# Optimization experiments

Measured on AMD Instinct MI355X. Metric: run time of the kernel, lower is better.

The kernel has to match this reference:

```python
import jax, jax.numpy as jnp
import numpy as np

N, D, H, E = 50000, 128, 128, 800000

def _layernorm(h, g, b, eps=1e-5):
    m = jnp.mean(h, axis=-1, keepdims=True)
    v = jnp.mean((h - m) ** 2, axis=-1, keepdims=True)
    return (h - m) * jax.lax.rsqrt(v + eps) * g + b

def setup_inputs() -> dict:
    key = jax.random.key(0)
    ks = jax.random.split(key, 24)
    s = 0.02
    inp = {
        "x": jax.random.normal(ks[0], (N, D), dtype=jnp.float32),
        "edge_index": jax.random.randint(ks[1], (2, E), 0, N, dtype=jnp.int64),
        "degree": jax.random.uniform(ks[2], (N, 1), dtype=jnp.float32) * 32.0,
        "W_lin": jax.random.normal(ks[3], (D, H), jnp.float32) * s,
        "b_lin": jnp.zeros((H,), jnp.float32),
        "Wa1": jax.random.normal(ks[4], (H, H), jnp.float32) * s,
        "ba1": jnp.zeros((H,), jnp.float32),
        "Wa2": jax.random.normal(ks[5], (H, H), jnp.float32) * s,
        "ba2": jnp.zeros((H,), jnp.float32),
        "Wb1": jax.random.normal(ks[6], (H, H), jnp.float32) * s,
        "bb1": jnp.zeros((H,), jnp.float32),
        "Wb2": jax.random.normal(ks[7], (H, H), jnp.float32) * s,
        "bb2": jnp.zeros((H,), jnp.float32),
        "Wg1": jax.random.normal(ks[8], (H, H), jnp.float32) * s,
        "bg1": jnp.zeros((H,), jnp.float32),
        "Wg2": jax.random.normal(ks[9], (H, H), jnp.float32) * s,
        "bg2": jnp.zeros((H,), jnp.float32),
        "Wf1": jax.random.normal(ks[10], (H, H), jnp.float32) * s,
        "bf1": jnp.zeros((H,), jnp.float32),
        "Wf2": jax.random.normal(ks[11], (H, H), jnp.float32) * s,
        "bf2": jnp.zeros((H,), jnp.float32),
        "ln_g": jnp.ones((H,), jnp.float32),
        "ln_b": jnp.zeros((H,), jnp.float32),
    }
    return inp

def reference(x, edge_index, degree, W_lin, b_lin, Wa1, ba1, Wa2, ba2,
              Wb1, bb1, Wb2, bb2, Wg1, bg1, Wg2, bg2, Wf1, bf1, Wf2, bf2,
              ln_g, ln_b):
    # Dropout layers are identity (eval mode)
    h = x @ W_lin + b_lin                                  # [N,H]
    x_res = _layernorm(h, ln_g, ln_b)
    alpha = jax.nn.softplus(jax.nn.relu(h @ Wa1 + ba1) @ Wa2 + ba2)
    beta = jax.nn.softplus(jax.nn.relu(h @ Wb1 + bb1) @ Wb2 + bb2)
    gamma = jax.nn.gelu(h @ Wg1 + bg1, approximate=False) @ Wg2 + bg2
    src, dst = edge_index[0], edge_index[1]
    agg = jax.ops.segment_sum(h[src], dst, num_segments=h.shape[0])  # [N,H]
    y = (beta * agg + gamma) / (alpha + beta * degree)
    z = jax.nn.gelu(y @ Wf1 + bf1, approximate=False) @ Wf2 + bf2
    return z + x_res
```

## Files before the change

### kernel.cpp

```cpp
#include <hip/hip_runtime.h>
#include <hip/hip_bf16.h>
#include <math.h>

#define NODES 50000
#define NEDGE 800000
#define NT_TILES 782
#define NBUCK 98
#define BSHIFT 9
#define BCAP 10240
#define NP1 195
#define EPB1 4104

typedef __bf16 bf16_t;
typedef __bf16 bf16x8 __attribute__((ext_vector_type(8)));
typedef float floatx4 __attribute__((ext_vector_type(4)));

__device__ __forceinline__ float bfbits2f(unsigned int hi16) {
    union { unsigned int u; float f; } c; c.u = hi16; return c.f;
}
__device__ __forceinline__ unsigned short f2bfbits(float f) {
    bf16_t b = (bf16_t)f; unsigned short u;
    __builtin_memcpy(&u, &b, 2); return u;
}

__device__ __forceinline__ float act_rt(float v, int act) {
    if (act == 1) return fmaxf(v, 0.f);
    if (act == 2) {
        float w = 0.79788456f * (v + 0.044715f * v * v * v);
        float e = __expf(2.f * w);
        float th = 1.f - 2.f / (e + 1.f);
        return 0.5f * v * (1.f + th);
    }
    if (act == 3) return fmaxf(v, 0.f) + __logf(1.f + __expf(-fabsf(v)));
    return v;
}

__global__ __launch_bounds__(256) void prep_w_zero(
    const float* __restrict__ w0, const float* __restrict__ w1,
    const float* __restrict__ w2, const float* __restrict__ w3,
    const float* __restrict__ w4, const float* __restrict__ w5,
    const float* __restrict__ w6, const float* __restrict__ w7,
    const float* __restrict__ w8, bf16_t* __restrict__ wt,
    int* __restrict__ gcur)
{
    if (blockIdx.x >= 9) {
        if (threadIdx.x < NBUCK) gcur[threadIdx.x] = 0;
        return;
    }
    const float* Ws[9] = {w0, w1, w2, w3, w4, w5, w6, w7, w8};
    const float* W = Ws[blockIdx.x];
    bf16_t* o = wt + blockIdx.x * 16384;
    for (int idx = threadIdx.x; idx < 16384; idx += 256) {
        int k = idx >> 7, n = idx & 127;
        o[n * 128 + k] = (bf16_t)W[idx];
    }
}

__device__ __forceinline__ void load_w_regs(const bf16_t* __restrict__ W,
                                            uint4 (&wr)[8], int t)
{
    for (int i = 0; i < 8; ++i) {
        int c = t + i * 256;
        int row = c >> 4, g = c & 15;
        wr[i] = *(const uint4*)(W + row * 128 + g * 8);
    }
}
__device__ __forceinline__ void store_w_regs(const uint4 (&wr)[8],
                                             bf16_t* Bs, int t)
{
    for (int i = 0; i < 8; ++i) {
        int c = t + i * 256;
        int row = c >> 4, g = c & 15;
        *(uint4*)&Bs[row * 128 + ((g ^ (row & 15)) * 8)] = wr[i];
    }
}
__device__ __forceinline__ void afrag_gbf16(const bf16_t* __restrict__ A,
        bf16x8 (&af)[4], int r0, int lane, int wave, int M)
{
    int gr = r0 + wave * 16 + (lane & 15);
    gr = min(gr, M - 1);
    const bf16_t* p = A + (size_t)gr * 128 + (lane >> 4) * 8;
    for (int kc = 0; kc < 4; ++kc)
        af[kc] = *(const bf16x8*)(p + kc * 32);
}
__device__ __forceinline__ void kloop64(const bf16x8 (&af)[4], const bf16_t* Bs,
                                        floatx4 (&acc)[8], int l15, int quad)
{
    for (int ni = 0; ni < 8; ++ni)
        for (int r = 0; r < 4; ++r) acc[ni][r] = 0.f;
    for (int kc = 0; kc < 4; ++kc) {
        int kg = kc * 4 + quad;
        bf16x8 b[8];
        for (int ni = 0; ni < 8; ++ni) {
            int row = ni * 16 + l15;
            b[ni] = *(const bf16x8*)&Bs[row * 128 + ((kg ^ l15) * 8)];
        }
        for (int ni = 0; ni < 8; ++ni)
            acc[ni] = __builtin_amdgcn_mfma_f32_16x16x32_bf16(
                af[kc], b[ni], acc[ni], 0, 0, 0);
    }
}
__device__ __forceinline__ void write_Csw(bf16_t* Csw, floatx4 (&acc)[8],
        const float (&bias_r)[8], int lane, int wave, int act)
{
    const int l15 = lane & 15, quad = lane >> 4;
    for (int ni = 0; ni < 8; ++ni) {
        int col = ni * 16 + l15;
        for (int r = 0; r < 4; ++r) {
            int row = wave * 16 + quad * 4 + r;
            float v = act_rt(acc[ni][r] + bias_r[ni], act);
            Csw[row * 128 + (((col >> 3) ^ (row & 15)) << 3) + (col & 7)] = (bf16_t)v;
        }
    }
}
__device__ __forceinline__ void afrag_Csw(const bf16_t* Csw, bf16x8 (&af)[4],
                                          int lane, int wave)
{
    int l15 = lane & 15, quad = lane >> 4;
    int row = wave * 16 + l15;
    for (int kc = 0; kc < 4; ++kc) {
        int kg = kc * 4 + quad;
        af[kc] = *(const bf16x8*)&Csw[row * 128 + ((kg ^ l15) * 8)];
    }
}
__device__ __forceinline__ void copy_Csw_out(const bf16_t* Csw,
        bf16_t* __restrict__ out, int t, int r0, int M)
{
    for (int i = 0; i < 4; ++i) {
        int c = t + i * 256;
        int row = c >> 4, g = c & 15;
        int gr = r0 + row;
        if (gr < M)
            *(uint4*)(out + (size_t)gr * 128 + g * 8) =
                *(const uint4*)&Csw[row * 128 + ((g ^ (row & 15)) * 8)];
    }
}

__global__ __launch_bounds__(256, 3) void hln_p1(
    const float* __restrict__ x, const bf16_t* __restrict__ wt,
    const float* __restrict__ b_lin,
    const float* __restrict__ ln_g, const float* __restrict__ ln_b,
    bf16_t* __restrict__ h, bf16_t* __restrict__ xres,
    const int* __restrict__ ei, int* __restrict__ gcur,
    unsigned* __restrict__ ebuf, int M)
{
    __shared__ __align__(16) char smem[49152];
    const int t = threadIdx.x;
    const int bid = blockIdx.x;

    if (bid % 5 == 4) {
        int* lcnt  = (int*)smem;
        int* lbase = lcnt + NBUCK;
        if (t < NBUCK) lcnt[t] = 0;
        __syncthreads();
        int p1id = bid / 5;
        int base = p1id * EPB1;
        int e_end = min(base + EPB1, NEDGE);
        for (int e = base + t; e < e_end; e += 256)
            atomicAdd(&lcnt[ei[NEDGE + e] >> BSHIFT], 1);
        __syncthreads();
        if (t < NBUCK) {
            lbase[t] = atomicAdd(&gcur[t], lcnt[t]);
            lcnt[t] = 0;
        }
        __syncthreads();
        for (int e = base + t; e < e_end; e += 256) {
            int d = ei[NEDGE + e];
            int s = ei[e];
            int b = d >> BSHIFT;
            int off = atomicAdd(&lcnt[b], 1);
            int pos = lbase[b] + off;
            if (pos < BCAP)
                ebuf[(size_t)b * BCAP + pos] =
                    (unsigned)s | ((unsigned)(d & 511) << 16);
        }
        return;
    }

    bf16_t* Bs  = (bf16_t*)smem;
    bf16_t* Csw = (bf16_t*)(smem + 32768);
    const int tile = bid - bid / 5;
    const int r0 = tile * 64;
    const int lane = t & 63, wave = t >> 6, l15 = lane & 15, quad = lane >> 4;
    uint4 wr[8];
    bf16x8 af[4];
    floatx4 acc[8];
    float bias_r[8];
    for (int ni = 0; ni < 8; ++ni) bias_r[ni] = b_lin[ni * 16 + l15];

    {
        int gr = min(r0 + wave * 16 + l15, M - 1);
        const float* p = x + (size_t)gr * 128 + quad * 8;
        for (int kc = 0; kc < 4; ++kc) {
            float4 u0 = *(const float4*)(p + kc * 32);
            float4 u1 = *(const float4*)(p + kc * 32 + 4);
            bf16x8 f;
            f[0] = (bf16_t)u0.x; f[1] = (bf16_t)u0.y;
            f[2] = (bf16_t)u0.z; f[3] = (bf16_t)u0.w;
            f[4] = (bf16_t)u1.x; f[5] = (bf16_t)u1.y;
            f[6] = (bf16_t)u1.z; f[7] = (bf16_t)u1.w;
            af[kc] = f;
        }
    }
    load_w_regs(wt, wr, t);
    store_w_regs(wr, Bs, t);
    __syncthreads();
    kloop64(af, Bs, acc, l15, quad);
    write_Csw(Csw, acc, bias_r, lane, wave, 0);
    __syncthreads();

    int row = t >> 2, p4 = t & 3;
    int gr = r0 + row;
    uint4 raw[4];
    float vals[32];
    float s = 0.f, sq = 0.f;
    for (int i = 0; i < 4; ++i) {
        int lg = p4 * 4 + i;
        raw[i] = *(const uint4*)&Csw[row * 128 + ((lg ^ (row & 15)) * 8)];
        const unsigned* u = (const unsigned*)&raw[i];
        for (int k = 0; k < 4; ++k) {
            float f0 = bfbits2f(u[k] << 16);
            float f1 = bfbits2f(u[k] & 0xffff0000u);
            vals[i * 8 + k * 2] = f0; vals[i * 8 + k * 2 + 1] = f1;
            s += f0 + f1; sq += f0 * f0 + f1 * f1;
        }
    }
    s += __shfl_xor(s, 1, 64);  sq += __shfl_xor(sq, 1, 64);
    s += __shfl_xor(s, 2, 64);  sq += __shfl_xor(sq, 2, 64);
    float m   = s * (1.f / 128.f);
    float var = fmaxf(sq * (1.f / 128.f) - m * m, 0.f);
    float rs  = rsqrtf(var + 1e-5f);
    if (gr < M) {
        for (int i = 0; i < 4; ++i) {
            int lg = p4 * 4 + i;
            *(uint4*)(h + (size_t)gr * 128 + lg * 8) = raw[i];
            unsigned short ob[8];
            for (int k = 0; k < 8; ++k) {
                int col = lg * 8 + k;
                ob[k] = f2bfbits((vals[i * 8 + k] - m) * rs * ln_g[col] + ln_b[col]);
            }
            uint4 o;
            o.x = ob[0] | ((unsigned)ob[1] << 16);
            o.y = ob[2] | ((unsigned)ob[3] << 16);
            o.z = ob[4] | ((unsigned)ob[5] << 16);
            o.w = ob[6] | ((unsigned)ob[7] << 16);
            *(uint4*)(xres + (size_t)gr * 128 + lg * 8) = o;
        }
    }
}

__global__ __launch_bounds__(256, 3) void branch_all(
    const bf16_t* __restrict__ h, const bf16_t* __restrict__ wt,
    const float* __restrict__ ba1, const float* __restrict__ ba2,
    const float* __restrict__ bb1, const float* __restrict__ bb2,
    const float* __restrict__ bg1, const float* __restrict__ bg2,
    bf16_t* __restrict__ al, bf16_t* __restrict__ be, bf16_t* __restrict__ ga,
    const int* __restrict__ gcur, const unsigned* __restrict__ ebuf,
    int* __restrict__ off_start, int* __restrict__ cntN,
    int* __restrict__ srcs, int M)
{
    __shared__ __align__(16) char smem[49152];
    const int t = threadIdx.x;
    const int bid = blockIdx.x;

    if (bid % 9 == 8) {
        int* ncnt = (int*)smem;
        int* sa   = ncnt + 512;
        int* sb   = sa + 512;
        int* ncur = sb + 512;
        int* red  = ncur + 512;
        const int b = bid / 9;
        if (b >= NBUCK) return;
        int total = min(gcur[b], BCAP);

        int v = 0;
        for (int j = t; j < b; j += 256) v += min(gcur[j], BCAP);
        for (int o = 1; o < 64; o <<= 1) v += __shfl_xor(v, o, 64);
        if ((t & 63) == 0) red[t >> 6] = v;
        ncnt[t] = 0; ncnt[t + 256] = 0;
        __syncthreads();
        int bucketBase = red[0] + red[1] + red[2] + red[3];

        const unsigned* eb = ebuf + (size_t)b * BCAP;
        for (int i = t; i < total; i += 256)
            atomicAdd(&ncnt[eb[i] >> 16], 1);
        __syncthreads();
        sa[t] = ncnt[t]; sa[t + 256] = ncnt[t + 256];
        __syncthreads();
        int* pin = sa; int* pout = sb;
        for (int o = 1; o < 512; o <<= 1) {
            for (int j = t; j < 512; j += 256)
                pout[j] = pin[j] + (j >= o ? pin[j - o] : 0);
            __syncthreads();
            int* tmp = pin; pin = pout; pout = tmp;
        }
        for (int j = t; j < 512; j += 256) {
            int excl = pin[j] - ncnt[j];
            int node = (b << BSHIFT) + j;
            if (node < NODES) {
                off_start[node] = bucketBase + excl;
                cntN[node] = ncnt[j];
            }
            ncur[j] = excl;
        }
        __syncthreads();
        for (int i = t; i < total; i += 256) {
            unsigned p = eb[i];
            int dl = p >> 16;
            int pos = atomicAdd(&ncur[dl], 1);
            srcs[bucketBase + pos] = (int)(p & 0xFFFFu);
        }
        return;
    }

    const int tile = bid - bid / 9;
    if (tile >= NT_TILES) return;
    bf16_t* Bs  = (bf16_t*)smem;
    bf16_t* Csw = (bf16_t*)(smem + 32768);
    const int r0 = tile * 64;
    const int lane = t & 63, wave = t >> 6, l15 = lane & 15, quad = lane >> 4;
    uint4 wr[8];
    bf16x8 af_h[4], af_t[4];
    floatx4 acc[8];
    float b1_r[8], b2_r[8];

    const float* B1s[3] = {ba1, bb1, bg1};
    const float* B2s[3] = {ba2, bb2, bg2};
    bf16_t* outs[3] = {al, be, ga};
    const int act1s[3] = {1, 1, 2};
    const int act2s[3] = {3, 3, 0};

    afrag_gbf16(h, af_h, r0, lane, wave, M);
    load_w_regs(wt + 1 * 16384, wr, t);

    #pragma unroll
    for (int b = 0; b < 3; ++b) {
        store_w_regs(wr, Bs, t);
        load_w_regs(wt + (2 + 2 * b) * 16384, wr, t);
        for (int ni = 0; ni < 8; ++ni) {
            b1_r[ni] = B1s[b][ni * 16 + l15];
            b2_r[ni] = B2s[b][ni * 16 + l15];
        }
        __syncthreads();
        kloop64(af_h, Bs, acc, l15, quad);
        write_Csw(Csw, acc, b1_r, lane, wave, act1s[b]);
        __syncthreads();
        store_w_regs(wr, Bs, t);
        afrag_Csw(Csw, af_t, lane, wave);
        if (b < 2)
            load_w_regs(wt + (3 + 2 * b) * 16384, wr, t);
        __syncthreads();
        kloop64(af_t, Bs, acc, l15, quad);
        __syncthreads();
        write_Csw(Csw, acc, b2_r, lane, wave, act2s[b]);
        __syncthreads();
        copy_Csw_out(Csw, outs[b], t, r0, M);
    }
}

__global__ __launch_bounds__(256) void gather_y_kernel(
    const int* __restrict__ off_start, const int* __restrict__ cnt,
    const int* __restrict__ srcs, const bf16_t* __restrict__ h,
    const bf16_t* __restrict__ al, const bf16_t* __restrict__ be,
    const bf16_t* __restrict__ ga, const float* __restrict__ deg,
    bf16_t* __restrict__ y, int M)
{
    int wave = threadIdx.x >> 6, lane = threadIdx.x & 63;
    int node = blockIdx.x * 4 + wave;
    if (node >= M) return;
    int s0 = __builtin_amdgcn_readfirstlane(off_start[node]);
    int n  = __builtin_amdgcn_readfirstlane(cnt[node]);
    int grp = lane >> 4, c16 = lane & 15;
    float a[8] = {0.f, 0.f, 0.f, 0.f, 0.f, 0.f, 0.f, 0.f};

    for (int j = 0; j < n; j += 16) {
        int idx[4];
        #pragma unroll
        for (int s = 0; s < 4; ++s)
            idx[s] = srcs[s0 + min(j + 4 * s + grp, n - 1)];
        uint4 v[4];
        #pragma unroll
        for (int s = 0; s < 4; ++s)
            v[s] = *(const uint4*)(h + (size_t)idx[s] * 128 + c16 * 8);
        #pragma unroll
        for (int s = 0; s < 4; ++s) {
            if (j + 4 * s + grp < n) {
                const unsigned* u = (const unsigned*)&v[s];
                #pragma unroll
                for (int k = 0; k < 4; ++k) {
                    a[2 * k]     += bfbits2f(u[k] << 16);
                    a[2 * k + 1] += bfbits2f(u[k] & 0xffff0000u);
                }
            }
        }
    }
    for (int k = 0; k < 8; ++k) {
        a[k] += __shfl_xor(a[k], 16, 64);
        a[k] += __shfl_xor(a[k], 32, 64);
    }
    if (lane < 16) {
        size_t i0 = (size_t)node * 128 + (size_t)c16 * 8;
        uint4 ra = *(const uint4*)(al + i0);
        uint4 rb = *(const uint4*)(be + i0);
        uint4 rg = *(const uint4*)(ga + i0);
        float d = deg[node];
        const unsigned* ua = (const unsigned*)&ra;
        const unsigned* ub = (const unsigned*)&rb;
        const unsigned* ug = (const unsigned*)&rg;
        unsigned short o[8];
        for (int k = 0; k < 4; ++k) {
            float a0 = bfbits2f(ua[k] << 16), a1 = bfbits2f(ua[k] & 0xffff0000u);
            float b0 = bfbits2f(ub[k] << 16), b1 = bfbits2f(ub[k] & 0xffff0000u);
            float g0 = bfbits2f(ug[k] << 16), g1 = bfbits2f(ug[k] & 0xffff0000u);
            o[2 * k]     = f2bfbits((b0 * a[2 * k]     + g0) / (a0 + b0 * d));
            o[2 * k + 1] = f2bfbits((b1 * a[2 * k + 1] + g1) / (a1 + b1 * d));
        }
        uint4 ov;
        ov.x = o[0] | ((unsigned)o[1] << 16);
        ov.y = o[2] | ((unsigned)o[3] << 16);
        ov.z = o[4] | ((unsigned)o[5] << 16);
        ov.w = o[6] | ((unsigned)o[7] << 16);
        *(uint4*)(y + i0) = ov;
    }
}

__global__ __launch_bounds__(256, 3) void fused_out(
    const bf16_t* __restrict__ y, const bf16_t* __restrict__ wt,
    const float* __restrict__ bf1, const float* __restrict__ bf2,
    const bf16_t* __restrict__ xres, float* __restrict__ out, int M)
{
    __shared__ __align__(16) char smem[49152];
    bf16_t* Bs  = (bf16_t*)smem;
    bf16_t* Csw = (bf16_t*)(smem + 32768);
    float*  Cf  = (float*)smem;
    const int t = threadIdx.x;
    const int r0 = blockIdx.x * 64;
    const int lane = t & 63, wave = t >> 6, l15 = lane & 15, quad = lane >> 4;
    uint4 wr[8];
    bf16x8 af[4];
    floatx4 acc[8];

    float b1_r[8], b2_r[8];
    for (int ni = 0; ni < 8; ++ni) {
        b1_r[ni] = bf1[ni * 16 + l15];
        b2_r[ni] = bf2[ni * 16 + l15];
    }

    afrag_gbf16(y, af, r0, lane, wave, M);
    load_w_regs(wt + 7 * 16384, wr, t);
    store_w_regs(wr, Bs, t);
    load_w_regs(wt + 8 * 16384, wr, t);
    __syncthreads();

    kloop64(af, Bs, acc, l15, quad);
    write_Csw(Csw, acc, b1_r, lane, wave, 2);
    __syncthreads();
    store_w_regs(wr, Bs, t);
    __syncthreads();

    afrag_Csw(Csw, af, lane, wave);
    kloop64(af, Bs, acc, l15, quad);
    __syncthreads();

    for (int ni = 0; ni < 8; ++ni) {
        int col = ni * 16 + l15;
        for (int r = 0; r < 4; ++r) {
            int row = wave * 16 + quad * 4 + r;
            Cf[row * 132 + col] = acc[ni][r] + b2_r[ni];
        }
    }
    __syncthreads();
    for (int i = 0; i < 8; ++i) {
        int c = t + i * 256;
        int row = c >> 5, q = c & 31;
        int gr = r0 + row;
        if (gr < M) {
            float4 v = *(const float4*)&Cf[row * 132 + q * 4];
            uint2 xr = *(const uint2*)(xres + (size_t)gr * 128 + q * 4);
            v.x += bfbits2f(xr.x << 16);
            v.y += bfbits2f(xr.x & 0xffff0000u);
            v.z += bfbits2f(xr.y << 16);
            v.w += bfbits2f(xr.y & 0xffff0000u);
            *(float4*)(out + (size_t)gr * 128 + q * 4) = v;
        }
    }
}

extern "C" void kernel_launch(void* const* d_in, const int* in_sizes, int n_in,
                              void* d_out, int out_size, void* d_ws, size_t ws_size,
                              hipStream_t stream)
{
    const float* x    = (const float*)d_in[0];
    const int*   ei   = (const int*)d_in[1];
    const float* deg  = (const float*)d_in[2];
    const float* W_lin = (const float*)d_in[3];  const float* b_lin = (const float*)d_in[4];
    const float* Wa1 = (const float*)d_in[5];    const float* ba1 = (const float*)d_in[6];
    const float* Wa2 = (const float*)d_in[7];    const float* ba2 = (const float*)d_in[8];
    const float* Wb1 = (const float*)d_in[9];    const float* bb1 = (const float*)d_in[10];
    const float* Wb2 = (const float*)d_in[11];   const float* bb2 = (const float*)d_in[12];
    const float* Wg1 = (const float*)d_in[13];   const float* bg1 = (const float*)d_in[14];
    const float* Wg2 = (const float*)d_in[15];   const float* bg2 = (const float*)d_in[16];
    const float* Wf1 = (const float*)d_in[17];   const float* bf1 = (const float*)d_in[18];
    const float* Wf2 = (const float*)d_in[19];   const float* bf2 = (const float*)d_in[20];
    const float* ln_g = (const float*)d_in[21];  const float* ln_b = (const float*)d_in[22];

    const int M = NODES;
    const size_t NB2 = (size_t)M * 128 * 2;

    char* ws = (char*)d_ws;
    size_t off = 0;
    bf16_t* wt  = (bf16_t*)(ws + off); off += (size_t)9 * 16384 * 2;
    bf16_t* h   = (bf16_t*)(ws + off); off += NB2;
    bf16_t* al  = (bf16_t*)(ws + off); off += NB2;
    bf16_t* be  = (bf16_t*)(ws + off); off += NB2;
    bf16_t* ga  = (bf16_t*)(ws + off); off += NB2;
    bf16_t* yv  = (bf16_t*)(ws + off); off += NB2;
    bf16_t* xres = (bf16_t*)(ws + off); off += NB2;
    int* gcur      = (int*)(ws + off); off += 128 * 4;
    int* off_start = (int*)(ws + off); off += (size_t)NODES * 4 + 64;
    int* cntN      = (int*)(ws + off); off += (size_t)NODES * 4 + 64;
    int* srcs      = (int*)(ws + off); off += (size_t)NEDGE * 4;
    unsigned* ebuf = (unsigned*)(ws + off); off += (size_t)NBUCK * BCAP * 4;
    float* outp = (float*)d_out;

    dim3 blk(256);

    prep_w_zero<<<10, blk, 0, stream>>>(
        W_lin, Wa1, Wa2, Wb1, Wb2, Wg1, Wg2, Wf1, Wf2, wt, gcur);

    hln_p1<<<977, blk, 0, stream>>>(
        x, wt, b_lin, ln_g, ln_b, h, xres, ei, gcur, ebuf, M);

    branch_all<<<891, blk, 0, stream>>>(
        h, wt, ba1, ba2, bb1, bb2, bg1, bg2, al, be, ga,
        gcur, ebuf, off_start, cntN, srcs, M);

    gather_y_kernel<<<(M + 3) / 4, blk, 0, stream>>>(off_start, cntN, srcs, h,
                                                     al, be, ga, deg, yv, M);
    fused_out<<<NT_TILES, blk, 0, stream>>>(yv, wt, bf1, bf2, xres, outp, M);
}
```

Before: 289.5 us.

## Read MFMA weight fragments directly from global memory instead of LDS staging

```diff
diff --git a/kernel.cpp b/kernel.cpp
--- a/kernel.cpp
+++ b/kernel.cpp
@@ -56,45 +56,31 @@
     }
 }
 
-__device__ __forceinline__ void load_w_regs(const bf16_t* __restrict__ W,
-                                            uint4 (&wr)[8], int t)
-{
-    for (int i = 0; i < 8; ++i) {
-        int c = t + i * 256;
-        int row = c >> 4, g = c & 15;
-        wr[i] = *(const uint4*)(W + row * 128 + g * 8);
-    }
-}
-__device__ __forceinline__ void store_w_regs(const uint4 (&wr)[8],
-                                             bf16_t* Bs, int t)
-{
-    for (int i = 0; i < 8; ++i) {
-        int c = t + i * 256;
-        int row = c >> 4, g = c & 15;
-        *(uint4*)&Bs[row * 128 + ((g ^ (row & 15)) * 8)] = wr[i];
-    }
-}
 __device__ __forceinline__ void afrag_gbf16(const bf16_t* __restrict__ A,
         bf16x8 (&af)[4], int r0, int lane, int wave, int M)
 {
     int gr = r0 + wave * 16 + (lane & 15);
     gr = min(gr, M - 1);
     const bf16_t* p = A + (size_t)gr * 128 + (lane >> 4) * 8;
+    #pragma unroll
     for (int kc = 0; kc < 4; ++kc)
         af[kc] = *(const bf16x8*)(p + kc * 32);
 }
-__device__ __forceinline__ void kloop64(const bf16x8 (&af)[4], const bf16_t* Bs,
-                                        floatx4 (&acc)[8], int l15, int quad)
-{
+__device__ __forceinline__ void kloop64g(const bf16x8 (&af)[4],
+        const bf16_t* __restrict__ W, floatx4 (&acc)[8], int l15, int quad)
+{
+    #pragma unroll
     for (int ni = 0; ni < 8; ++ni)
+        #pragma unroll
         for (int r = 0; r < 4; ++r) acc[ni][r] = 0.f;
+    #pragma unroll
     for (int kc = 0; kc < 4; ++kc) {
         int kg = kc * 4 + quad;
         bf16x8 b[8];
-        for (int ni = 0; ni < 8; ++ni) {
-            int row = ni * 16 + l15;
-            b[ni] = *(const bf16x8*)&Bs[row * 128 + ((kg ^ l15) * 8)];
-        }
+        #pragma unroll
+        for (int ni = 0; ni < 8; ++ni)
+            b[ni] = *(const bf16x8*)(W + (ni * 16 + l15) * 128 + kg * 8);
+        #pragma unroll
         for (int ni = 0; ni < 8; ++ni)
             acc[ni] = __builtin_amdgcn_mfma_f32_16x16x32_bf16(
                 af[kc], b[ni], acc[ni], 0, 0, 0);
@@ -104,8 +90,10 @@
         const float (&bias_r)[8], int lane, int wave, int act)
 {
     const int l15 = lane & 15, quad = lane >> 4;
+    #pragma unroll
     for (int ni = 0; ni < 8; ++ni) {
         int col = ni * 16 + l15;
+        #pragma unroll
         for (int r = 0; r < 4; ++r) {
             int row = wave * 16 + quad * 4 + r;
             float v = act_rt(acc[ni][r] + bias_r[ni], act);
@@ -118,6 +106,7 @@
 {
     int l15 = lane & 15, quad = lane >> 4;
     int row = wave * 16 + l15;
+    #pragma unroll
     for (int kc = 0; kc < 4; ++kc) {
         int kg = kc * 4 + quad;
         af[kc] = *(const bf16x8*)&Csw[row * 128 + ((kg ^ l15) * 8)];
@@ -126,6 +115,7 @@
 __device__ __forceinline__ void copy_Csw_out(const bf16_t* Csw,
         bf16_t* __restrict__ out, int t, int r0, int M)
 {
+    #pragma unroll
     for (int i = 0; i < 4; ++i) {
         int c = t + i * 256;
         int row = c >> 4, g = c & 15;
@@ -136,7 +126,7 @@
     }
 }
 
-__global__ __launch_bounds__(256, 3) void hln_p1(
+__global__ __launch_bounds__(256, 4) void hln_p1(
     const float* __restrict__ x, const bf16_t* __restrict__ wt,
     const float* __restrict__ b_lin,
     const float* __restrict__ ln_g, const float* __restrict__ ln_b,
@@ -144,7 +134,7 @@
     const int* __restrict__ ei, int* __restrict__ gcur,
     unsigned* __restrict__ ebuf, int M)
 {
-    __shared__ __align__(16) char smem[49152];
+    __shared__ __align__(16) char smem[16384];
     const int t = threadIdx.x;
     const int bid = blockIdx.x;
 
@@ -177,12 +167,10 @@
         return;
     }
 
-    bf16_t* Bs  = (bf16_t*)smem;
-    bf16_t* Csw = (bf16_t*)(smem + 32768);
+    bf16_t* Csw = (bf16_t*)smem;
     const int tile = bid - bid / 5;
     const int r0 = tile * 64;
     const int lane = t & 63, wave = t >> 6, l15 = lane & 15, quad = lane >> 4;
-    uint4 wr[8];
     bf16x8 af[4];
     floatx4 acc[8];
     float bias_r[8];
@@ -191,6 +179,7 @@
     {
         int gr = min(r0 + wave * 16 + l15, M - 1);
         const float* p = x + (size_t)gr * 128 + quad * 8;
+        #pragma unroll
         for (int kc = 0; kc < 4; ++kc) {
             float4 u0 = *(const float4*)(p + kc * 32);
             float4 u1 = *(const float4*)(p + kc * 32 + 4);
@@ -202,10 +191,7 @@
             af[kc] = f;
         }
     }
-    load_w_regs(wt, wr, t);
-    store_w_regs(wr, Bs, t);
-    __syncthreads();
-    kloop64(af, Bs, acc, l15, quad);
+    kloop64g(af, wt, acc, l15, quad);
     write_Csw(Csw, acc, bias_r, lane, wave, 0);
     __syncthreads();
 
@@ -249,7 +235,7 @@
     }
 }
 
-__global__ __launch_bounds__(256, 3) void branch_all(
+__global__ __launch_bounds__(256, 4) void branch_all(
     const bf16_t* __restrict__ h, const bf16_t* __restrict__ wt,
     const float* __restrict__ ba1, const float* __restrict__ ba2,
     const float* __restrict__ bb1, const float* __restrict__ bb2,
@@ -259,7 +245,7 @@
     int* __restrict__ off_start, int* __restrict__ cntN,
     int* __restrict__ srcs, int M)
 {
-    __shared__ __align__(16) char smem[49152];
+    __shared__ __align__(16) char smem[16384];
     const int t = threadIdx.x;
     const int bid = blockIdx.x;
 
@@ -315,11 +301,9 @@
 
     const int tile = bid - bid / 9;
     if (tile >= NT_TILES) return;
-    bf16_t* Bs  = (bf16_t*)smem;
-    bf16_t* Csw = (bf16_t*)(smem + 32768);
+    bf16_t* Csw = (bf16_t*)smem;
     const int r0 = tile * 64;
     const int lane = t & 63, wave = t >> 6, l15 = lane & 15, quad = lane >> 4;
-    uint4 wr[8];
     bf16x8 af_h[4], af_t[4];
     floatx4 acc[8];
     float b1_r[8], b2_r[8];
@@ -331,30 +315,21 @@
     const int act2s[3] = {3, 3, 0};
 
     afrag_gbf16(h, af_h, r0, lane, wave, M);
-    load_w_regs(wt + 1 * 16384, wr, t);
 
     #pragma unroll
     for (int b = 0; b < 3; ++b) {
-        store_w_regs(wr, Bs, t);
-        load_w_regs(wt + (2 + 2 * b) * 16384, wr, t);
         for (int ni = 0; ni < 8; ++ni) {
             b1_r[ni] = B1s[b][ni * 16 + l15];
             b2_r[ni] = B2s[b][ni * 16 + l15];
         }
-        __syncthreads();
-        kloop64(af_h, Bs, acc, l15, quad);
+        kloop64g(af_h, wt + (1 + 2 * b) * 16384, acc, l15, quad);
         write_Csw(Csw, acc, b1_r, lane, wave, act1s[b]);
-        __syncthreads();
-        store_w_regs(wr, Bs, t);
         afrag_Csw(Csw, af_t, lane, wave);
-        if (b < 2)
-            load_w_regs(wt + (3 + 2 * b) * 16384, wr, t);
-        __syncthreads();
-        kloop64(af_t, Bs, acc, l15, quad);
-        __syncthreads();
+        kloop64g(af_t, wt + (2 + 2 * b) * 16384, acc, l15, quad);
         write_Csw(Csw, acc, b2_r, lane, wave, act2s[b]);
         __syncthreads();
         copy_Csw_out(Csw, outs[b], t, r0, M);
+        __syncthreads();
     }
 }
 
@@ -424,19 +399,17 @@
     }
 }
 
-__global__ __launch_bounds__(256, 3) void fused_out(
+__global__ __launch_bounds__(256, 4) void fused_out(
     const bf16_t* __restrict__ y, const bf16_t* __restrict__ wt,
     const float* __restrict__ bf1, const float* __restrict__ bf2,
     const bf16_t* __restrict__ xres, float* __restrict__ out, int M)
 {
-    __shared__ __align__(16) char smem[49152];
-    bf16_t* Bs  = (bf16_t*)smem;
-    bf16_t* Csw = (bf16_t*)(smem + 32768);
+    __shared__ __align__(16) char smem[33792];
+    bf16_t* Csw = (bf16_t*)smem;
     float*  Cf  = (float*)smem;
     const int t = threadIdx.x;
     const int r0 = blockIdx.x * 64;
     const int lane = t & 63, wave = t >> 6, l15 = lane & 15, quad = lane >> 4;
-    uint4 wr[8];
     bf16x8 af[4];
     floatx4 acc[8];
 
@@ -447,20 +420,11 @@
     }
 
     afrag_gbf16(y, af, r0, lane, wave, M);
-    load_w_regs(wt + 7 * 16384, wr, t);
-    store_w_regs(wr, Bs, t);
-    load_w_regs(wt + 8 * 16384, wr, t);
+    kloop64g(af, wt + 7 * 16384, acc, l15, quad);
+    write_Csw(Csw, acc, b1_r, lane, wave, 2);
+    afrag_Csw(Csw, af, lane, wave);
     __syncthreads();
-
-    kloop64(af, Bs, acc, l15, quad);
-    write_Csw(Csw, acc, b1_r, lane, wave, 2);
-    __syncthreads();
-    store_w_regs(wr, Bs, t);
-    __syncthreads();
-
-    afrag_Csw(Csw, af, lane, wave);
-    kloop64(af, Bs, acc, l15, quad);
-    __syncthreads();
+    kloop64g(af, wt + 8 * 16384, acc, l15, quad);
 
     for (int ni = 0; ni < 8; ++ni) {
         int col = ni * 16 + l15;
```

Result: slower. 338.6 us (+16.9%).
